# Optimization experiments

Hardware: AMD Instinct MI355X
Metric: run time of the kernel (lower is better)

Reference implementation:

```python
import jax, jax.numpy as jnp
import numpy as np

B, S, D, H = 4, 2048, 1024, 16
HD = D // H  # head_dim = 64


def setup_inputs() -> dict:
    key = jax.random.key(0)
    ks = jax.random.split(key, 5)
    scale = 0.02
    x = jax.random.normal(ks[0], (B, S, D), dtype=jnp.float32)
    W_qkv = jax.random.normal(ks[1], (D, 3 * D), dtype=jnp.float32) * scale
    b_qkv = jnp.zeros((3 * D,), dtype=jnp.float32)
    W_out = jax.random.normal(ks[2], (D, D), dtype=jnp.float32) * scale
    b_out = jnp.zeros((D,), dtype=jnp.float32)
    return {"x": x, "W_qkv": W_qkv, "b_qkv": b_qkv, "W_out": W_out, "b_out": b_out}


def reference(x, W_qkv, b_qkv, W_out, b_out):
    b, s, d = x.shape
    qkv = x @ W_qkv + b_qkv                      # [B,S,3D]
    q, k, v = jnp.split(qkv, 3, axis=-1)
    # [B,S,D] -> [B,H,S,hd]
    q = q.reshape(b, s, H, HD).transpose(0, 2, 1, 3)
    k = k.reshape(b, s, H, HD).transpose(0, 2, 1, 3)
    v = v.reshape(b, s, H, HD).transpose(0, 2, 1, 3)
    scores = jnp.einsum('bhqd,bhkd->bhqk', q, k) / jnp.sqrt(jnp.float32(HD))
    causal = jnp.tril(jnp.ones((s, s), dtype=bool))  # [S,S]
    scores = jnp.where(causal[None, None], scores, -jnp.inf)
    probs = jax.nn.softmax(scores, axis=-1)
    # dropout is identity in eval mode
    attn = jnp.einsum('bhqk,bhkd->bhqd', probs, v)  # [B,H,S,hd]
    attn = attn.transpose(0, 2, 1, 3).reshape(b, s, d)
    return attn @ W_out + b_out
```

## Files before the change

### kernel.cpp

```cpp
#include <hip/hip_runtime.h>


typedef short s16;
typedef __attribute__((ext_vector_type(4))) short s16x4;
typedef __attribute__((ext_vector_type(8))) short bf16x8;
typedef __attribute__((ext_vector_type(4))) float f32x4;

__device__ __forceinline__ s16 f2bf(float f) {
    union { float f; unsigned int i; } v;
    v.f = f;
    unsigned int r = v.i + 0x7fffu + ((v.i >> 16) & 1u);
    return (s16)(r >> 16);
}

__device__ __forceinline__ unsigned pack_bf16(float a, float b) {
    union { float f; unsigned u; } x, y;
    x.f = a; y.f = b;
    return __byte_perm(x.u + 0x8000u, y.u + 0x8000u, 0x7632);
}

__device__ __forceinline__ void load_lds16(const s16* g, s16* lds_base) {
    __builtin_amdgcn_global_load_lds(
        (const __attribute__((address_space(1))) void*)g,
        (__attribute__((address_space(3))) void*)lds_base, 16, 0, 0);
}

__global__ void cast_f32_bf16(const float* __restrict__ in, s16* __restrict__ out) {
    const int i = (blockIdx.x * 256 + threadIdx.x) * 4;
    const float4 f = *(const float4*)(in + i);
    s16x4 r = {f2bf(f.x), f2bf(f.y), f2bf(f.z), f2bf(f.w)};
    *(s16x4*)(out + i) = r;
}

__global__ void transpose_cast(const float* __restrict__ in,
                               s16* __restrict__ out, int R, int C) {
    __shared__ float tile[32][33];
    const int cb = blockIdx.x * 32, rb = blockIdx.y * 32;
    const int tx = threadIdx.x, ty = threadIdx.y;
#pragma unroll
    for (int i = 0; i < 32; i += 8)
        tile[ty + i][tx] = in[(size_t)(rb + ty + i) * C + cb + tx];
    __syncthreads();
#pragma unroll
    for (int i = 0; i < 32; i += 8)
        out[(size_t)(cb + ty + i) * R + rb + tx] = f2bf(tile[tx][ty + i]);
}

template <bool OUT_F32>
__global__ __launch_bounds__(512, 2) void gemm_bt_bias_8p(
    const s16* __restrict__ A,
    const s16* __restrict__ Bt,
    const float* __restrict__ bias,
    void* __restrict__ Cv,
    int M, int N, int K) {
    __shared__ __attribute__((aligned(16))) s16 As[2][128 * 64];
    __shared__ __attribute__((aligned(16))) s16 Bs[2][256 * 64];

    const int tid  = threadIdx.x;
    const int lane = tid & 63;
    const int wave = tid >> 6;
    const int l15  = lane & 15;
    const int quad = lane >> 4;
    const int wr   = wave >> 2;
    const int wc   = wave & 3;
    const int m0 = blockIdx.y * 128;
    const int n0 = blockIdx.x * 256;

    const int srow = tid >> 3;
    const int sg   = (tid & 7) ^ (srow & 7);
    const s16* Ag = A  + (size_t)(m0 + srow) * K + sg * 8;
    const s16* Bg = Bt + (size_t)(n0 + srow) * K + sg * 8;

#define STAGE_A8(buf, h, kt) load_lds16(Ag + (size_t)(h) * 64 * K + (size_t)(kt) * 64, \
                                        &As[buf][(h) * 4096 + wave * 512])
#define STAGE_B8(buf, u, kt) load_lds16(Bg + (size_t)(u) * 64 * K + (size_t)(kt) * 64, \
                                        &Bs[buf][(u) * 4096 + wave * 512])

    f32x4 acc[4][4];
#pragma unroll
    for (int i = 0; i < 4; ++i)
#pragma unroll
        for (int j = 0; j < 4; ++j)
            acc[i][j] = (f32x4){0.f, 0.f, 0.f, 0.f};

    const int nk = K >> 6;

    STAGE_A8(0, 0, 0); STAGE_A8(0, 1, 0);
    STAGE_B8(0, 0, 0); STAGE_B8(0, 1, 0); STAGE_B8(0, 2, 0); STAGE_B8(0, 3, 0);
    __syncthreads();

    for (int t = 0; t < nk; ++t) {
        const int buf  = t & 1;
        const int nbuf = buf ^ 1;
        const bool pre = (t + 1 < nk);
#pragma unroll
        for (int p = 0; p < 4; ++p) {
            const int mh = p >> 1, nh = p & 1;
            bf16x8 af[2][2], bfr[2][2];
#pragma unroll
            for (int i = 0; i < 2; ++i)
#pragma unroll
                for (int ks = 0; ks < 2; ++ks) {
                    const int ar = wr * 64 + (mh * 2 + i) * 16 + l15;
                    const int br = wc * 64 + (nh * 2 + i) * 16 + l15;
                    const int gs = ((ks * 4 + quad) ^ (l15 & 7)) * 8;
                    af[i][ks]  = *(const bf16x8*)(&As[buf][ar * 64 + gs]);
                    bfr[i][ks] = *(const bf16x8*)(&Bs[buf][br * 64 + gs]);
                }
            if (p == 0 && pre) {
                STAGE_A8(nbuf, 0, t + 1); STAGE_A8(nbuf, 1, t + 1);
                STAGE_B8(nbuf, 0, t + 1);
            }
            if (p == 1 && pre) {
                STAGE_B8(nbuf, 1, t + 1); STAGE_B8(nbuf, 2, t + 1);
                STAGE_B8(nbuf, 3, t + 1);
            }
            __builtin_amdgcn_s_barrier();
            __builtin_amdgcn_s_setprio(1);
#pragma unroll
            for (int i = 0; i < 2; ++i)
#pragma unroll
                for (int j = 0; j < 2; ++j)
#pragma unroll
                    for (int ks = 0; ks < 2; ++ks)
                        acc[mh * 2 + i][nh * 2 + j] = __builtin_amdgcn_mfma_f32_16x16x32_bf16(
                            af[i][ks], bfr[j][ks], acc[mh * 2 + i][nh * 2 + j], 0, 0, 0);
            __builtin_amdgcn_s_setprio(0);
            if (p == 3)
                __syncthreads();
            else
                __builtin_amdgcn_s_barrier();
        }
    }
#undef STAGE_A8
#undef STAGE_B8

#pragma unroll
    for (int nt = 0; nt < 4; ++nt) {
        const int col = n0 + wc * 64 + nt * 16 + l15;
        const float bv = bias[col];
#pragma unroll
        for (int mt = 0; mt < 4; ++mt) {
            const int rowb = m0 + wr * 64 + mt * 16 + quad * 4;
#pragma unroll
            for (int r = 0; r < 4; ++r) {
                const float v = acc[mt][nt][r] + bv;
                if constexpr (OUT_F32)
                    ((float*)Cv)[(size_t)(rowb + r) * N + col] = v;
                else
                    ((s16*)Cv)[(size_t)(rowb + r) * N + col] = f2bf(v);
            }
        }
    }
}

__global__ __launch_bounds__(256) void attn_fwd(
    const s16* __restrict__ qkv,
    s16* __restrict__ attn) {
    __shared__ __attribute__((aligned(16))) s16 Ks[64 * 72];
    __shared__ __attribute__((aligned(16))) s16 Vt[64 * 72];
    __shared__ __attribute__((aligned(16))) s16 PT[4][32][88];

    const int tid  = threadIdx.x;
    const int lane = tid & 63;
    const int wave = tid >> 6;
    const int l15  = lane & 15;
    const int quad = lane >> 4;

    const int bid = blockIdx.x;
    const int hi  = bid >> 8;
    const int a   = bid & 3;
    const int bh  = (bid >> 2) & 63;
    const int qbase = a * 2 + (hi >> 1);
    const int qt  = (hi & 1) ? 15 - qbase : qbase;

    const size_t rowbase = (size_t)(bh >> 4) * 2048;
    const int hoff = (bh & 15) * 64;
    const int kp  = tid >> 3;
    const int p_s = tid & 7;
    const int kg  = kp >> 2;

    const float C2 = 0.18033688011112042f;
    const float M2 = 12.0f;

    const int wq = qt * 128 + wave * 32;

    bf16x8 qf[2][2];
#pragma unroll
    for (int qs = 0; qs < 2; ++qs)
#pragma unroll
        for (int ks = 0; ks < 2; ++ks)
            qf[qs][ks] = *(const bf16x8*)(qkv + (rowbase + wq + qs * 16 + l15) * 3072 + hoff + ks * 32 + quad * 8);

    float l_lane[2] = {0.f, 0.f};
    f32x4 o[2][4];
#pragma unroll
    for (int qs = 0; qs < 2; ++qs)
#pragma unroll
        for (int hs = 0; hs < 4; ++hs)
            o[qs][hs] = (f32x4){0.f, 0.f, 0.f, 0.f};

    const int nkt = qt * 2 + 2;
    bf16x8 kv[2], vv[2];
#pragma unroll
    for (int dk = 0; dk < 2; ++dk) {
        const s16* g = qkv + (rowbase + 2 * kp + dk) * 3072 + hoff + p_s * 8;
        kv[dk] = *(const bf16x8*)(g + 1024);
        vv[dk] = *(const bf16x8*)(g + 2048);
    }

    for (int kt = 0; kt < nkt; ++kt) {
        const int k0 = kt * 64;
        __syncthreads();
#pragma unroll
        for (int dk = 0; dk < 2; ++dk)
            *(bf16x8*)(Ks + (2 * kp + dk) * 72 + p_s * 8) = kv[dk];
#pragma unroll
        for (int j = 0; j < 8; ++j) {
            const unsigned dw = (unsigned)(unsigned short)vv[0][j] |
                                ((unsigned)(unsigned short)vv[1][j] << 16);
            *(unsigned*)(Vt + (p_s * 8 + j) * 72 + ((kg ^ p_s) << 3) + (2 * kp & 7)) = dw;
        }
        __syncthreads();

        if (kt + 1 < nkt) {
#pragma unroll
            for (int dk = 0; dk < 2; ++dk) {
                const s16* g = qkv + (rowbase + k0 + 64 + 2 * kp + dk) * 3072 + hoff + p_s * 8;
                kv[dk] = *(const bf16x8*)(g + 1024);
                vv[dk] = *(const bf16x8*)(g + 2048);
            }
        }

        if (k0 > wq + 31) continue;

        f32x4 st[2][4];
#pragma unroll
        for (int qs = 0; qs < 2; ++qs)
#pragma unroll
            for (int kb = 0; kb < 4; ++kb)
                st[qs][kb] = (f32x4){0.f, 0.f, 0.f, 0.f};
        __builtin_amdgcn_s_setprio(1);
#pragma unroll
        for (int kb = 0; kb < 4; ++kb)
#pragma unroll
            for (int ks = 0; ks < 2; ++ks) {
                const bf16x8 kf = *(const bf16x8*)(Ks + (kb * 16 + l15) * 72 + ks * 32 + quad * 8);
#pragma unroll
                for (int qs = 0; qs < 2; ++qs)
                    st[qs][kb] = __builtin_amdgcn_mfma_f32_16x16x32_bf16(kf, qf[qs][ks], st[qs][kb], 0, 0, 0);
            }
        __builtin_amdgcn_s_setprio(0);

        const bool edge = (k0 + 63 > wq);
#pragma unroll
        for (int qs = 0; qs < 2; ++qs) {
            const int q = wq + qs * 16 + l15;
#pragma unroll
            for (int kb = 0; kb < 4; ++kb) {
                float p4[4];
#pragma unroll
                for (int r = 0; r < 4; ++r) {
                    float t = fmaf(st[qs][kb][r], C2, -M2);
                    if (edge) {
                        const int key = k0 + kb * 16 + quad * 4 + r;
                        t = (key <= q) ? t : -150.f;
                    }
                    p4[r] = __builtin_amdgcn_exp2f(t);
                    l_lane[qs] += p4[r];
                }
                uint2 dd;
                dd.x = pack_bf16(p4[0], p4[1]);
                dd.y = pack_bf16(p4[2], p4[3]);
                *(uint2*)(&PT[wave][qs * 16 + l15][kb * 16 + quad * 4]) = dd;
            }
        }

        __builtin_amdgcn_s_setprio(1);
#pragma unroll
        for (int kk = 0; kk < 2; ++kk) {
            bf16x8 pf[2];
#pragma unroll
            for (int qs = 0; qs < 2; ++qs)
                pf[qs] = *(const bf16x8*)(&PT[wave][qs * 16 + l15][kk * 32 + quad * 8]);
#pragma unroll
            for (int hs = 0; hs < 4; ++hs) {
                const bf16x8 vf = *(const bf16x8*)(
                    Vt + (hs * 16 + l15) * 72 + (((kk * 4 + quad) ^ (2 * hs + (l15 >> 3))) << 3));
#pragma unroll
                for (int qs = 0; qs < 2; ++qs)
                    o[qs][hs] = __builtin_amdgcn_mfma_f32_16x16x32_bf16(vf, pf[qs], o[qs][hs], 0, 0, 0);
            }
        }
        __builtin_amdgcn_s_setprio(0);
    }

    float rl[2];
#pragma unroll
    for (int qs = 0; qs < 2; ++qs) {
        float l = l_lane[qs];
        l += __shfl_xor(l, 16);
        l += __shfl_xor(l, 32);
        rl[qs] = 1.f / l;
    }

#pragma unroll
    for (int qs = 0; qs < 2; ++qs) {
        const int q = wq + qs * 16 + l15;
#pragma unroll
        for (int hs = 0; hs < 4; ++hs) {
            uint2 dd;
            dd.x = pack_bf16(o[qs][hs][0] * rl[qs], o[qs][hs][1] * rl[qs]);
            dd.y = pack_bf16(o[qs][hs][2] * rl[qs], o[qs][hs][3] * rl[qs]);
            *(uint2*)(attn + (rowbase + q) * 1024 + hoff + hs * 16 + quad * 4) = dd;
        }
    }
}

extern "C" void kernel_launch(void* const* d_in, const int* in_sizes, int n_in,
                              void* d_out, int out_size, void* d_ws, size_t ws_size,
                              hipStream_t stream) {
    const float* x    = (const float*)d_in[0];
    const float* Wqkv = (const float*)d_in[1];
    const float* bqkv = (const float*)d_in[2];
    const float* Wout = (const float*)d_in[3];
    const float* bout = (const float*)d_in[4];
    float* out = (float*)d_out;

    s16* ws   = (s16*)d_ws;
    s16* qkv  = ws;
    s16* xba  = qkv + (size_t)8192 * 3072;
    s16* wtq  = xba + (size_t)8192 * 1024;
    s16* wto  = wtq + (size_t)3072 * 1024;

    cast_f32_bf16<<<8192, 256, 0, stream>>>(x, xba);
    transpose_cast<<<dim3(3072 / 32, 1024 / 32), dim3(32, 8), 0, stream>>>(Wqkv, wtq, 1024, 3072);
    transpose_cast<<<dim3(1024 / 32, 1024 / 32), dim3(32, 8), 0, stream>>>(Wout, wto, 1024, 1024);
    gemm_bt_bias_8p<false><<<dim3(3072 / 256, 8192 / 128), 512, 0, stream>>>(
        xba, wtq, bqkv, qkv, 8192, 3072, 1024);
    attn_fwd<<<1024, 256, 0, stream>>>(qkv, xba);
    gemm_bt_bias_8p<true><<<dim3(1024 / 256, 8192 / 128), 512, 0, stream>>>(
        xba, wto, bout, out, 8192, 1024, 1024);
}
```

Measured before the change: 269.0 us.

## Enlarge GEMM tiles to 256x256 with block-id swizzle for XCD locality

Changes the bf16 GEMM block tile from 128x256 to 256x256. Each wave now computes 128x64 with B fragments loaded once per k-step and reused across four M sub-steps, which cuts LDS reads and global traffic per FLOP. It also moves to a 1D grid with a modulo-8 block-id swizzle so that neighbouring tiles land on the same XCD and share L2. The costs are LDS growing to 128KB per block, double the accumulator registers, and fewer blocks (384 and 128), which risks lower occupancy and poor wave balance on the output GEMM.

```diff
diff --git a/kernel.cpp b/kernel.cpp
--- a/kernel.cpp
+++ b/kernel.cpp
@@ -47,13 +47,13 @@
 }
 
 template <bool OUT_F32>
-__global__ __launch_bounds__(512, 2) void gemm_bt_bias_8p(
+__global__ __launch_bounds__(512, 2) void gemm_bt_bias_256(
     const s16* __restrict__ A,
     const s16* __restrict__ Bt,
     const float* __restrict__ bias,
     void* __restrict__ Cv,
-    int M, int N, int K) {
-    __shared__ __attribute__((aligned(16))) s16 As[2][128 * 64];
+    int M, int N, int K, int gx) {
+    __shared__ __attribute__((aligned(16))) s16 As[2][256 * 64];
     __shared__ __attribute__((aligned(16))) s16 Bs[2][256 * 64];
 
     const int tid  = threadIdx.x;
@@ -63,88 +63,93 @@
     const int quad = lane >> 4;
     const int wr   = wave >> 2;
     const int wc   = wave & 3;
-    const int m0 = blockIdx.y * 128;
-    const int n0 = blockIdx.x * 256;
+
+    const int cpx = (int)gridDim.x >> 3;
+    const int bid = (int)blockIdx.x;
+    const int swz = (bid & 7) * cpx + (bid >> 3);
+    const int m0 = (swz / gx) * 256;
+    const int n0 = (swz % gx) * 256;
 
     const int srow = tid >> 3;
     const int sg   = (tid & 7) ^ (srow & 7);
     const s16* Ag = A  + (size_t)(m0 + srow) * K + sg * 8;
     const s16* Bg = Bt + (size_t)(n0 + srow) * K + sg * 8;
 
-#define STAGE_A8(buf, h, kt) load_lds16(Ag + (size_t)(h) * 64 * K + (size_t)(kt) * 64, \
-                                        &As[buf][(h) * 4096 + wave * 512])
-#define STAGE_B8(buf, u, kt) load_lds16(Bg + (size_t)(u) * 64 * K + (size_t)(kt) * 64, \
-                                        &Bs[buf][(u) * 4096 + wave * 512])
-
-    f32x4 acc[4][4];
-#pragma unroll
-    for (int i = 0; i < 4; ++i)
+#define STG(buf, c, kt) do {                                                        \
+    load_lds16(Ag + (size_t)(c) * 64 * K + (size_t)(kt) * 64,                       \
+               &As[buf][(c) * 4096 + wave * 512]);                                  \
+    load_lds16(Bg + (size_t)(c) * 64 * K + (size_t)(kt) * 64,                       \
+               &Bs[buf][(c) * 4096 + wave * 512]); } while (0)
+
+    f32x4 acc[8][4];
+#pragma unroll
+    for (int i = 0; i < 8; ++i)
 #pragma unroll
         for (int j = 0; j < 4; ++j)
             acc[i][j] = (f32x4){0.f, 0.f, 0.f, 0.f};
 
     const int nk = K >> 6;
 
-    STAGE_A8(0, 0, 0); STAGE_A8(0, 1, 0);
-    STAGE_B8(0, 0, 0); STAGE_B8(0, 1, 0); STAGE_B8(0, 2, 0); STAGE_B8(0, 3, 0);
+    STG(0, 0, 0); STG(0, 1, 0); STG(0, 2, 0); STG(0, 3, 0);
     __syncthreads();
 
     for (int t = 0; t < nk; ++t) {
         const int buf  = t & 1;
         const int nbuf = buf ^ 1;
         const bool pre = (t + 1 < nk);
-#pragma unroll
-        for (int p = 0; p < 4; ++p) {
-            const int mh = p >> 1, nh = p & 1;
-            bf16x8 af[2][2], bfr[2][2];
+        bf16x8 bfr[4][2];
+#pragma unroll
+        for (int q = 0; q < 4; ++q) {
+            if (q == 0) {
+#pragma unroll
+                for (int n = 0; n < 4; ++n)
+#pragma unroll
+                    for (int ks = 0; ks < 2; ++ks) {
+                        const int br = wc * 64 + n * 16 + l15;
+                        const int gs = ((ks * 4 + quad) ^ (l15 & 7)) * 8;
+                        bfr[n][ks] = *(const bf16x8*)(&Bs[buf][br * 64 + gs]);
+                    }
+            }
+            bf16x8 af[2][2];
 #pragma unroll
             for (int i = 0; i < 2; ++i)
 #pragma unroll
                 for (int ks = 0; ks < 2; ++ks) {
-                    const int ar = wr * 64 + (mh * 2 + i) * 16 + l15;
-                    const int br = wc * 64 + (nh * 2 + i) * 16 + l15;
+                    const int ar = wr * 128 + (q * 2 + i) * 16 + l15;
                     const int gs = ((ks * 4 + quad) ^ (l15 & 7)) * 8;
-                    af[i][ks]  = *(const bf16x8*)(&As[buf][ar * 64 + gs]);
-                    bfr[i][ks] = *(const bf16x8*)(&Bs[buf][br * 64 + gs]);
+                    af[i][ks] = *(const bf16x8*)(&As[buf][ar * 64 + gs]);
                 }
-            if (p == 0 && pre) {
-                STAGE_A8(nbuf, 0, t + 1); STAGE_A8(nbuf, 1, t + 1);
-                STAGE_B8(nbuf, 0, t + 1);
-            }
-            if (p == 1 && pre) {
-                STAGE_B8(nbuf, 1, t + 1); STAGE_B8(nbuf, 2, t + 1);
-                STAGE_B8(nbuf, 3, t + 1);
-            }
+            if (q == 0 && pre) { STG(nbuf, 0, t + 1); STG(nbuf, 1, t + 1); }
+            if (q == 1 && pre) { STG(nbuf, 2, t + 1); STG(nbuf, 3, t + 1); }
             __builtin_amdgcn_s_barrier();
             __builtin_amdgcn_s_setprio(1);
 #pragma unroll
             for (int i = 0; i < 2; ++i)
 #pragma unroll
-                for (int j = 0; j < 2; ++j)
+                for (int n = 0; n < 4; ++n)
 #pragma unroll
                     for (int ks = 0; ks < 2; ++ks)
-                        acc[mh * 2 + i][nh * 2 + j] = __builtin_amdgcn_mfma_f32_16x16x32_bf16(
-                            af[i][ks], bfr[j][ks], acc[mh * 2 + i][nh * 2 + j], 0, 0, 0);
+                        acc[q * 2 + i][n] = __builtin_amdgcn_mfma_f32_16x16x32_bf16(
+                            af[i][ks], bfr[n][ks], acc[q * 2 + i][n], 0, 0, 0);
             __builtin_amdgcn_s_setprio(0);
-            if (p == 3)
+            if (q == 3)
                 __syncthreads();
             else
                 __builtin_amdgcn_s_barrier();
         }
     }
-#undef STAGE_A8
-#undef STAGE_B8
-
-#pragma unroll
-    for (int nt = 0; nt < 4; ++nt) {
-        const int col = n0 + wc * 64 + nt * 16 + l15;
+#undef STG
+
+#pragma unroll
+    for (int n = 0; n < 4; ++n) {
+        const int col = n0 + wc * 64 + n * 16 + l15;
         const float bv = bias[col];
 #pragma unroll
-        for (int mt = 0; mt < 4; ++mt) {
-            const int rowb = m0 + wr * 64 + mt * 16 + quad * 4;
+        for (int mf = 0; mf < 8; ++mf) {
+            const int rowb = m0 + wr * 128 + mf * 16 + quad * 4;
 #pragma unroll
             for (int r = 0; r < 4; ++r) {
-                const float v = acc[mt][nt][r] + bv;
+                const float v = acc[mf][n][r] + bv;
                 if constexpr (OUT_F32)
                     ((float*)Cv)[(size_t)(rowb + r) * N + col] = v;
                 else
@@ -336,9 +341,9 @@
     cast_f32_bf16<<<8192, 256, 0, stream>>>(x, xba);
     transpose_cast<<<dim3(3072 / 32, 1024 / 32), dim3(32, 8), 0, stream>>>(Wqkv, wtq, 1024, 3072);
     transpose_cast<<<dim3(1024 / 32, 1024 / 32), dim3(32, 8), 0, stream>>>(Wout, wto, 1024, 1024);
-    gemm_bt_bias_8p<false><<<dim3(3072 / 256, 8192 / 128), 512, 0, stream>>>(
-        xba, wtq, bqkv, qkv, 8192, 3072, 1024);
+    gemm_bt_bias_256<false><<<384, 512, 0, stream>>>(
+        xba, wtq, bqkv, qkv, 8192, 3072, 1024, 12);
     attn_fwd<<<1024, 256, 0, stream>>>(qkv, xba);
-    gemm_bt_bias_8p<true><<<dim3(1024 / 256, 8192 / 128), 512, 0, stream>>>(
-        xba, wto, bout, out, 8192, 1024, 1024);
-}
+    gemm_bt_bias_256<true><<<128, 512, 0, stream>>>(
+        xba, wto, bout, out, 8192, 1024, 1024, 4);
+}
```

New measurement: 268.8 us. Within noise of the previous version (-0.1%).
